# Kernel tuning notes

Measured on AMD Instinct MI355X. Metric: run time of the kernel, lower is better.

## Reference

```python
import jax, jax.numpy as jnp
import numpy as np

N_NODES = 100000
N_EDGES = 1600000
D_IN = 64
H = 64


def setup_inputs() -> dict:
    key = jax.random.key(0)
    ks = jax.random.split(key, 8)
    inp = {
        "x": jax.random.normal(ks[0], (N_NODES, D_IN), dtype=jnp.float32),
        "edge_index": jax.random.randint(ks[1], (2, N_EDGES), 0, N_NODES, dtype=jnp.int64),
        # layer 1 (SAGEConv): lin_l (aggregated neighbors, with bias), lin_r (root, no bias)
        "Wl1": jax.random.normal(ks[2], (D_IN, H), dtype=jnp.float32) / np.sqrt(D_IN),
        "bl1": jnp.zeros((H,), dtype=jnp.float32),
        "Wr1": jax.random.normal(ks[3], (D_IN, H), dtype=jnp.float32) / np.sqrt(D_IN),
        # layer 2
        "Wl2": jax.random.normal(ks[4], (H, H), dtype=jnp.float32) / np.sqrt(H),
        "bl2": jnp.zeros((H,), dtype=jnp.float32),
        "Wr2": jax.random.normal(ks[5], (H, H), dtype=jnp.float32) / np.sqrt(H),
        "Wfc": jax.random.normal(ks[6], (H, 1), dtype=jnp.float32) / np.sqrt(H),
        "bfc": jnp.zeros((1,), dtype=jnp.float32),
    }
    return inp


def _sage_conv(h, src, dst, inv_deg, Wl, bl, Wr):
    # mean-aggregate neighbor features: scatter-add messages then normalize by in-degree
    agg = jax.ops.segment_sum(h[src], dst, num_segments=N_NODES)  # [N, d]
    agg = agg * inv_deg[:, None]
    return agg @ Wl + bl + h @ Wr


def reference(x, edge_index, Wl1, bl1, Wr1, Wl2, bl2, Wr2, Wfc, bfc):
    src, dst = edge_index[0], edge_index[1]
    deg = jax.ops.segment_sum(jnp.ones((src.shape[0],), dtype=x.dtype), dst,
                              num_segments=N_NODES)
    inv_deg = jnp.where(deg > 0, 1.0 / jnp.maximum(deg, 1.0), 0.0)

    h = jax.nn.relu(_sage_conv(x, src, dst, inv_deg, Wl1, bl1, Wr1))
    h = jax.nn.relu(_sage_conv(h, src, dst, inv_deg, Wl2, bl2, Wr2))
    return h @ Wfc + bfc  # [N, 1]
```

## Files before the change

### kernel.cpp

```cpp
#include <hip/hip_runtime.h>
#include <hip/hip_fp16.h>

#define NN 100000
#define NE 1600000
#define SHIFT 8
#define NBUCK 391
#define P1B   391
#define EPB   4093

typedef _Float16 f16x8 __attribute__((ext_vector_type(8)));
typedef float f32x4 __attribute__((ext_vector_type(4)));
union H8U4 { f16x8 h; uint4 u; };

__global__ __launch_bounds__(256) void k_to_f16(const float4* __restrict__ in, ushort4* __restrict__ out, int n4) {
    int i = blockIdx.x * 256 + threadIdx.x;
    if (i < n4) {
        float4 f = in[i];
        _Float16 a = (_Float16)f.x, b = (_Float16)f.y, c = (_Float16)f.z, d = (_Float16)f.w;
        ushort4 u;
        u.x = *(unsigned short*)&a; u.y = *(unsigned short*)&b;
        u.z = *(unsigned short*)&c; u.w = *(unsigned short*)&d;
        out[i] = u;
    }
}

__global__ __launch_bounds__(256) void k_prep_w(const float* __restrict__ Wl, const float* __restrict__ Wr,
                                                unsigned short* __restrict__ wt) {
    int idx = blockIdx.x * 256 + threadIdx.x;
    if (idx < 64 * 128) {
        int n = idx >> 7, k = idx & 127;
        float v = (k < 64) ? Wl[k * 64 + n] : Wr[(k - 64) * 64 + n];
        _Float16 h = (_Float16)v;
        wt[idx] = *(unsigned short*)&h;
    }
}

__global__ __launch_bounds__(256) void k_p1_hist(const int* __restrict__ dst, int* __restrict__ hist) {
    __shared__ int h[NBUCK];
    int t = threadIdx.x, blk = blockIdx.x;
    for (int i = t; i < NBUCK; i += 256) h[i] = 0;
    __syncthreads();
    int beg = blk * EPB, end = min(beg + EPB, NE);
    for (int e = beg + t; e < end; e += 256) atomicAdd(&h[dst[e] >> SHIFT], 1);
    __syncthreads();
    for (int i = t; i < NBUCK; i += 256) hist[(size_t)i * P1B + blk] = h[i];
}

__global__ __launch_bounds__(256) void k_bin_total(const int* __restrict__ hist, int* __restrict__ bin_total) {
    __shared__ int sd[256];
    int b = blockIdx.x, t = threadIdx.x;
    int v = 0;
    for (int i = t; i < P1B; i += 256) v += hist[(size_t)b * P1B + i];
    sd[t] = v;
    __syncthreads();
    for (int s = 128; s > 0; s >>= 1) {
        if (t < s) sd[t] += sd[t + s];
        __syncthreads();
    }
    if (t == 0) bin_total[b] = sd[0];
}

__global__ __launch_bounds__(512) void k_bin_base(const int* __restrict__ bin_total, int* __restrict__ bucket_start,
                                                  int* __restrict__ offsets) {
    __shared__ int s[512];
    int t = threadIdx.x;
    int v = (t < NBUCK) ? bin_total[t] : 0;
    s[t] = v;
    __syncthreads();
    for (int off = 1; off < 512; off <<= 1) {
        int add = (t >= off) ? s[t - off] : 0;
        __syncthreads();
        s[t] += add;
        __syncthreads();
    }
    if (t < NBUCK) bucket_start[t] = s[t] - v;
    if (t == 0) { bucket_start[NBUCK] = NE; offsets[NN] = NE; }
}

__global__ __launch_bounds__(512) void k_cursor_base(int* __restrict__ hist, const int* __restrict__ bucket_start) {
    __shared__ int s[512];
    int b = blockIdx.x, t = threadIdx.x;
    int v = (t < P1B) ? hist[(size_t)b * P1B + t] : 0;
    s[t] = v;
    __syncthreads();
    for (int off = 1; off < 512; off <<= 1) {
        int add = (t >= off) ? s[t - off] : 0;
        __syncthreads();
        s[t] += add;
        __syncthreads();
    }
    if (t < P1B) hist[(size_t)b * P1B + t] = bucket_start[b] + s[t] - v;
}

__global__ __launch_bounds__(256) void k_p1_scatter(const int* __restrict__ src, const int* __restrict__ dst,
                                                    const int* __restrict__ hist, unsigned int* __restrict__ pairs) {
    __shared__ int cur[NBUCK];
    int t = threadIdx.x, blk = blockIdx.x;
    for (int i = t; i < NBUCK; i += 256) cur[i] = hist[(size_t)i * P1B + blk];
    __syncthreads();
    int beg = blk * EPB, end = min(beg + EPB, NE);
    for (int e = beg + t; e < end; e += 256) {
        int d = dst[e];
        int pos = atomicAdd(&cur[d >> SHIFT], 1);
        pairs[pos] = (unsigned int)src[e] | ((unsigned int)(d & 255) << 17);
    }
}

__global__ __launch_bounds__(256) void k_bucket_csr(const unsigned int* __restrict__ pairs,
                                                    const int* __restrict__ bucket_start,
                                                    int* __restrict__ ssrc, int* __restrict__ offsets,
                                                    float* __restrict__ inv_deg) {
    __shared__ int cnt[256];
    __shared__ int excl[256];
    int b = blockIdx.x, t = threadIdx.x;
    cnt[t] = 0;
    __syncthreads();
    int beg = bucket_start[b], end = bucket_start[b + 1];
    for (int e = beg + t; e < end; e += 256) atomicAdd(&cnt[pairs[e] >> 17], 1);
    __syncthreads();
    int deg = cnt[t];
    excl[t] = deg;
    __syncthreads();
    for (int off = 1; off < 256; off <<= 1) {
        int add = (t >= off) ? excl[t - off] : 0;
        __syncthreads();
        excl[t] += add;
        __syncthreads();
    }
    int ex = excl[t] - deg;
    int node = (b << SHIFT) + t;
    if (node < NN) {
        offsets[node] = beg + ex;
        inv_deg[node] = (deg > 0) ? (1.0f / (float)deg) : 0.0f;
    }
    __syncthreads();
    cnt[t] = beg + ex;
    __syncthreads();
    for (int e = beg + t; e < end; e += 256) {
        unsigned int pr = pairs[e];
        int pos = atomicAdd(&cnt[pr >> 17], 1);
        ssrc[pos] = (int)(pr & 0x1FFFFu);
    }
}

__global__ __launch_bounds__(256) void k_aggregate(const uint4* __restrict__ featq,
                                                   const int* __restrict__ ssrc,
                                                   const int* __restrict__ offsets, const float* __restrict__ inv_deg,
                                                   uint4* __restrict__ outq) {
    int node = blockIdx.x * 4 + (threadIdx.x >> 6);
    int lane = threadIdx.x & 63;
    if (node >= NN) return;
    int c = lane & 7, g = lane >> 3;
    int beg = offsets[node], end = offsets[node + 1];
    H8U4 acc;
    acc.h = (f16x8)(_Float16)0;
    int e = beg;

    for (; e + 16 <= end; e += 16) {
        int i0 = ssrc[e + g];
        int i1 = ssrc[e + 8 + g];
        H8U4 q0, q1;
        q0.u = featq[(size_t)i0 * 8 + c];
        q1.u = featq[(size_t)i1 * 8 + c];
        acc.h += q0.h;
        acc.h += q1.h;
    }
    for (; e < end; e += 8) {
        int m = end - e;
        int idx = ssrc[e + (g < m ? g : m - 1)];
        H8U4 q;
        q.u = featq[(size_t)idx * 8 + c];
        if (g < m) acc.h += q.h;
    }

#pragma unroll
    for (int mask = 8; mask <= 32; mask <<= 1) {
        H8U4 o;
        o.u.x = __shfl_xor(acc.u.x, mask);
        o.u.y = __shfl_xor(acc.u.y, mask);
        o.u.z = __shfl_xor(acc.u.z, mask);
        o.u.w = __shfl_xor(acc.u.w, mask);
        acc.h += o.h;
    }

    if (g == 0) {
        float s = inv_deg[node];
        H8U4 r;
#pragma unroll
        for (int j = 0; j < 8; j++) r.h[j] = (_Float16)((float)acc.h[j] * s);
        outq[(size_t)node * 8 + c] = r.u;
    }
}

template <bool FUSE_HEAD>
__global__ __launch_bounds__(256) void k_linear(const uint4* __restrict__ aggq, const uint4* __restrict__ rootq,
                                                const uint4* __restrict__ wtq,
                                                const float* __restrict__ bias,
                                                const float* __restrict__ Wfc, const float* __restrict__ bfc,
                                                float* __restrict__ out_f32, unsigned short* __restrict__ out_f16) {
    int tid = threadIdx.x;
    int wave = tid >> 6, lane = tid & 63;
    int nb = blockIdx.x * 64 + wave * 16;
    int m = lane & 15, quad = lane >> 4;

    int an = nb + m;
    if (an > NN - 1) an = NN - 1;
    H8U4 a[4];
    a[0].u = aggq[(size_t)an * 8 + quad];
    a[1].u = aggq[(size_t)an * 8 + 4 + quad];
    a[2].u = rootq[(size_t)an * 8 + quad];
    a[3].u = rootq[(size_t)an * 8 + 4 + quad];

    f32x4 acc[4];
#pragma unroll
    for (int n = 0; n < 4; n++) acc[n] = (f32x4){0.f, 0.f, 0.f, 0.f};

#pragma unroll
    for (int ncol = 0; ncol < 4; ncol++) {
        int col = ncol * 16 + m;
#pragma unroll
        for (int ki = 0; ki < 4; ki++) {
            H8U4 b;
            b.u = wtq[col * 16 + ki * 4 + quad];
            acc[ncol] = __builtin_amdgcn_mfma_f32_16x16x32_f16(a[ki].h, b.h, acc[ncol], 0, 0, 0);
        }
    }

    float bs[4];
#pragma unroll
    for (int ncol = 0; ncol < 4; ncol++) bs[ncol] = bias[ncol * 16 + m];

    if (!FUSE_HEAD) {
#pragma unroll
        for (int r = 0; r < 4; r++) {
            int node = nb + quad * 4 + r;
            if (node < NN) {
#pragma unroll
                for (int ncol = 0; ncol < 4; ncol++) {
                    float v = fmaxf(acc[ncol][r] + bs[ncol], 0.f);
                    _Float16 hv = (_Float16)v;
                    out_f16[(size_t)node * 64 + ncol * 16 + m] = *(unsigned short*)&hv;
                }
            }
        }
    } else {
        float wf[4];
#pragma unroll
        for (int ncol = 0; ncol < 4; ncol++) wf[ncol] = Wfc[ncol * 16 + m];
#pragma unroll
        for (int r = 0; r < 4; r++) {
            int node = nb + quad * 4 + r;
            float partial = 0.f;
#pragma unroll
            for (int ncol = 0; ncol < 4; ncol++)
                partial += fmaxf(acc[ncol][r] + bs[ncol], 0.f) * wf[ncol];
            partial += __shfl_xor(partial, 1);
            partial += __shfl_xor(partial, 2);
            partial += __shfl_xor(partial, 4);
            partial += __shfl_xor(partial, 8);
            if (m == 0 && node < NN) out_f32[node] = partial + bfc[0];
        }
    }
}

extern "C" void kernel_launch(void* const* d_in, const int* in_sizes, int n_in,
                              void* d_out, int out_size, void* d_ws, size_t ws_size,
                              hipStream_t stream) {
    const float* x   = (const float*)d_in[0];
    const int*   ei  = (const int*)d_in[1];
    const float* Wl1 = (const float*)d_in[2];
    const float* bl1 = (const float*)d_in[3];
    const float* Wr1 = (const float*)d_in[4];
    const float* Wl2 = (const float*)d_in[5];
    const float* bl2 = (const float*)d_in[6];
    const float* Wr2 = (const float*)d_in[7];
    const float* Wfc = (const float*)d_in[8];
    const float* bfc = (const float*)d_in[9];
    float* out = (float*)d_out;

    const int* src = ei;
    const int* dst = ei + NE;

    char* p = (char*)d_ws;
    auto carve = [&](size_t bytes) {
        char* q = p;
        p += (bytes + 255) & ~size_t(255);
        return q;
    };
    int*            offsets = (int*)carve((size_t)(NN + 1) * 4);
    float*          inv_deg = (float*)carve((size_t)NN * 4);
    int*            ssrc    = (int*)carve((size_t)NE * 4);
    unsigned short* xh      = (unsigned short*)carve((size_t)NN * 64 * 2);
    unsigned short* h1h     = (unsigned short*)carve((size_t)NN * 64 * 2);
    unsigned short* aggh    = (unsigned short*)carve((size_t)NN * 64 * 2);
    unsigned short* wt1     = (unsigned short*)carve(64 * 128 * 2);
    unsigned short* wt2     = (unsigned short*)carve(64 * 128 * 2);
    unsigned int* pairs        = (unsigned int*)aggh;
    int*          hist         = (int*)(pairs + NE);
    int*          bin_total    = hist + (size_t)NBUCK * P1B;
    int*          bucket_start = bin_total + NBUCK;

    const int n4   = NN * 64 / 4;
    const int tile = (NN + 63) / 64;

    k_to_f16<<<(n4 + 255) / 256, 256, 0, stream>>>((const float4*)x, (ushort4*)xh, n4);
    k_prep_w<<<32, 256, 0, stream>>>(Wl1, Wr1, wt1);
    k_prep_w<<<32, 256, 0, stream>>>(Wl2, Wr2, wt2);

    k_p1_hist<<<P1B, 256, 0, stream>>>(dst, hist);
    k_bin_total<<<NBUCK, 256, 0, stream>>>(hist, bin_total);
    k_bin_base<<<1, 512, 0, stream>>>(bin_total, bucket_start, offsets);
    k_cursor_base<<<NBUCK, 512, 0, stream>>>(hist, bucket_start);
    k_p1_scatter<<<P1B, 256, 0, stream>>>(src, dst, hist, pairs);
    k_bucket_csr<<<NBUCK, 256, 0, stream>>>(pairs, bucket_start, ssrc, offsets, inv_deg);

    k_aggregate<<<(NN + 3) / 4, 256, 0, stream>>>((const uint4*)xh, ssrc, offsets, inv_deg, (uint4*)aggh);
    k_linear<false><<<tile, 256, 0, stream>>>((const uint4*)aggh, (const uint4*)xh, (const uint4*)wt1,
                                              bl1, Wfc, bfc, nullptr, h1h);
    k_aggregate<<<(NN + 3) / 4, 256, 0, stream>>>((const uint4*)h1h, ssrc, offsets, inv_deg, (uint4*)aggh);
    k_linear<true><<<tile, 256, 0, stream>>>((const uint4*)aggh, (const uint4*)h1h, (const uint4*)wt2,
                                             bl2, Wfc, bfc, out, nullptr);
}
```

Baseline: 260.4 us.

## Fuse CSR build and f16 prep into one cooperative kernel with grid syncs

Replaces nine separate preprocessing launches (f16 conversion, weight transposes, histogram, bin totals, scans, scatter, bucket CSR) with a single cooperative kernel of 391 blocks that uses grid.sync between phases. The aim is to remove per-launch overhead and idle gaps between small dependent kernels. The cost is a cooperative launch that needs all 391 blocks resident at once, grid-wide barriers, and f16 conversion spread over fewer blocks, each doing a larger share.

```diff
diff --git a/kernel.cpp b/kernel.cpp
--- a/kernel.cpp
+++ b/kernel.cpp
@@ -1,5 +1,8 @@
 #include <hip/hip_runtime.h>
 #include <hip/hip_fp16.h>
+#include <hip/hip_cooperative_groups.h>
+
+namespace cg = cooperative_groups;
 
 #define NN 100000
 #define NE 1600000
@@ -12,134 +15,139 @@
 typedef float f32x4 __attribute__((ext_vector_type(4)));
 union H8U4 { f16x8 h; uint4 u; };
 
-__global__ __launch_bounds__(256) void k_to_f16(const float4* __restrict__ in, ushort4* __restrict__ out, int n4) {
-    int i = blockIdx.x * 256 + threadIdx.x;
-    if (i < n4) {
-        float4 f = in[i];
-        _Float16 a = (_Float16)f.x, b = (_Float16)f.y, c = (_Float16)f.z, d = (_Float16)f.w;
-        ushort4 u;
-        u.x = *(unsigned short*)&a; u.y = *(unsigned short*)&b;
-        u.z = *(unsigned short*)&c; u.w = *(unsigned short*)&d;
-        out[i] = u;
-    }
-}
-
-__global__ __launch_bounds__(256) void k_prep_w(const float* __restrict__ Wl, const float* __restrict__ Wr,
-                                                unsigned short* __restrict__ wt) {
-    int idx = blockIdx.x * 256 + threadIdx.x;
-    if (idx < 64 * 128) {
-        int n = idx >> 7, k = idx & 127;
-        float v = (k < 64) ? Wl[k * 64 + n] : Wr[(k - 64) * 64 + n];
-        _Float16 h = (_Float16)v;
-        wt[idx] = *(unsigned short*)&h;
-    }
-}
-
-__global__ __launch_bounds__(256) void k_p1_hist(const int* __restrict__ dst, int* __restrict__ hist) {
-    __shared__ int h[NBUCK];
-    int t = threadIdx.x, blk = blockIdx.x;
-    for (int i = t; i < NBUCK; i += 256) h[i] = 0;
-    __syncthreads();
-    int beg = blk * EPB, end = min(beg + EPB, NE);
-    for (int e = beg + t; e < end; e += 256) atomicAdd(&h[dst[e] >> SHIFT], 1);
-    __syncthreads();
-    for (int i = t; i < NBUCK; i += 256) hist[(size_t)i * P1B + blk] = h[i];
-}
-
-__global__ __launch_bounds__(256) void k_bin_total(const int* __restrict__ hist, int* __restrict__ bin_total) {
-    __shared__ int sd[256];
-    int b = blockIdx.x, t = threadIdx.x;
-    int v = 0;
-    for (int i = t; i < P1B; i += 256) v += hist[(size_t)b * P1B + i];
-    sd[t] = v;
-    __syncthreads();
-    for (int s = 128; s > 0; s >>= 1) {
-        if (t < s) sd[t] += sd[t + s];
-        __syncthreads();
-    }
-    if (t == 0) bin_total[b] = sd[0];
-}
-
-__global__ __launch_bounds__(512) void k_bin_base(const int* __restrict__ bin_total, int* __restrict__ bucket_start,
-                                                  int* __restrict__ offsets) {
-    __shared__ int s[512];
-    int t = threadIdx.x;
-    int v = (t < NBUCK) ? bin_total[t] : 0;
+__device__ __forceinline__ int scan256(int* s, int t, int v) {
     s[t] = v;
     __syncthreads();
-    for (int off = 1; off < 512; off <<= 1) {
+    for (int off = 1; off < 256; off <<= 1) {
         int add = (t >= off) ? s[t - off] : 0;
         __syncthreads();
         s[t] += add;
         __syncthreads();
     }
-    if (t < NBUCK) bucket_start[t] = s[t] - v;
-    if (t == 0) { bucket_start[NBUCK] = NE; offsets[NN] = NE; }
-}
-
-__global__ __launch_bounds__(512) void k_cursor_base(int* __restrict__ hist, const int* __restrict__ bucket_start) {
-    __shared__ int s[512];
-    int b = blockIdx.x, t = threadIdx.x;
-    int v = (t < P1B) ? hist[(size_t)b * P1B + t] : 0;
-    s[t] = v;
-    __syncthreads();
-    for (int off = 1; off < 512; off <<= 1) {
-        int add = (t >= off) ? s[t - off] : 0;
-        __syncthreads();
-        s[t] += add;
-        __syncthreads();
-    }
-    if (t < P1B) hist[(size_t)b * P1B + t] = bucket_start[b] + s[t] - v;
-}
-
-__global__ __launch_bounds__(256) void k_p1_scatter(const int* __restrict__ src, const int* __restrict__ dst,
-                                                    const int* __restrict__ hist, unsigned int* __restrict__ pairs) {
-    __shared__ int cur[NBUCK];
-    int t = threadIdx.x, blk = blockIdx.x;
-    for (int i = t; i < NBUCK; i += 256) cur[i] = hist[(size_t)i * P1B + blk];
-    __syncthreads();
-    int beg = blk * EPB, end = min(beg + EPB, NE);
-    for (int e = beg + t; e < end; e += 256) {
-        int d = dst[e];
-        int pos = atomicAdd(&cur[d >> SHIFT], 1);
-        pairs[pos] = (unsigned int)src[e] | ((unsigned int)(d & 255) << 17);
-    }
-}
-
-__global__ __launch_bounds__(256) void k_bucket_csr(const unsigned int* __restrict__ pairs,
-                                                    const int* __restrict__ bucket_start,
-                                                    int* __restrict__ ssrc, int* __restrict__ offsets,
-                                                    float* __restrict__ inv_deg) {
-    __shared__ int cnt[256];
-    __shared__ int excl[256];
-    int b = blockIdx.x, t = threadIdx.x;
-    cnt[t] = 0;
-    __syncthreads();
-    int beg = bucket_start[b], end = bucket_start[b + 1];
-    for (int e = beg + t; e < end; e += 256) atomicAdd(&cnt[pairs[e] >> 17], 1);
-    __syncthreads();
-    int deg = cnt[t];
-    excl[t] = deg;
-    __syncthreads();
-    for (int off = 1; off < 256; off <<= 1) {
-        int add = (t >= off) ? excl[t - off] : 0;
-        __syncthreads();
-        excl[t] += add;
-        __syncthreads();
-    }
-    int ex = excl[t] - deg;
-    int node = (b << SHIFT) + t;
-    if (node < NN) {
-        offsets[node] = beg + ex;
-        inv_deg[node] = (deg > 0) ? (1.0f / (float)deg) : 0.0f;
-    }
-    __syncthreads();
-    cnt[t] = beg + ex;
-    __syncthreads();
-    for (int e = beg + t; e < end; e += 256) {
-        unsigned int pr = pairs[e];
-        int pos = atomicAdd(&cnt[pr >> 17], 1);
-        ssrc[pos] = (int)(pr & 0x1FFFFu);
+    return s[t];
+}
+
+__global__ __launch_bounds__(256) void k_build(
+    const float4* __restrict__ x4, ushort4* __restrict__ xh4,
+    const float* __restrict__ Wl1, const float* __restrict__ Wr1, unsigned short* __restrict__ wt1,
+    const float* __restrict__ Wl2, const float* __restrict__ Wr2, unsigned short* __restrict__ wt2,
+    const int* __restrict__ src, const int* __restrict__ dst,
+    int* __restrict__ hist, int* __restrict__ bin_total, int* __restrict__ bucket_start,
+    unsigned int* __restrict__ pairs, int* __restrict__ ssrc,
+    int* __restrict__ offsets, float* __restrict__ inv_deg)
+{
+    cg::grid_group grid = cg::this_grid();
+    __shared__ int sA[NBUCK];
+    __shared__ int sS[256];
+    __shared__ int sX[256];
+    int blk = blockIdx.x, t = threadIdx.x;
+
+    {
+        const int n4 = NN * 16;
+        const int per = (n4 + P1B - 1) / P1B;
+        int cb = blk * per, ce = min(cb + per, n4);
+        for (int i = cb + t; i < ce; i += 256) {
+            float4 f = x4[i];
+            _Float16 a = (_Float16)f.x, b = (_Float16)f.y, c = (_Float16)f.z, d = (_Float16)f.w;
+            ushort4 u;
+            u.x = *(unsigned short*)&a; u.y = *(unsigned short*)&b;
+            u.z = *(unsigned short*)&c; u.w = *(unsigned short*)&d;
+            xh4[i] = u;
+        }
+        if (blk < 64) {
+            int idx = (blk & 31) * 256 + t;
+            const float* Wl = (blk < 32) ? Wl1 : Wl2;
+            const float* Wr = (blk < 32) ? Wr1 : Wr2;
+            unsigned short* wt = (blk < 32) ? wt1 : wt2;
+            int n = idx >> 7, k = idx & 127;
+            float v = (k < 64) ? Wl[k * 64 + n] : Wr[(k - 64) * 64 + n];
+            _Float16 h = (_Float16)v;
+            wt[idx] = *(unsigned short*)&h;
+        }
+        for (int i = t; i < NBUCK; i += 256) sA[i] = 0;
+        __syncthreads();
+        int eb = blk * EPB, ee = min(eb + EPB, NE);
+        for (int e = eb + t; e < ee; e += 256) atomicAdd(&sA[dst[e] >> SHIFT], 1);
+        __syncthreads();
+        for (int i = t; i < NBUCK; i += 256) hist[(size_t)i * P1B + blk] = sA[i];
+    }
+    grid.sync();
+
+    {
+        int v = 0;
+        for (int i = t; i < P1B; i += 256) v += hist[(size_t)blk * P1B + i];
+        sS[t] = v;
+        __syncthreads();
+        for (int s = 128; s > 0; s >>= 1) {
+            if (t < s) sS[t] += sS[t + s];
+            __syncthreads();
+        }
+        if (t == 0) bin_total[blk] = sS[0];
+    }
+    grid.sync();
+
+    if (blk == 0) {
+        int v0 = bin_total[t];
+        int incl0 = scan256(sS, t, v0);
+        bucket_start[t] = incl0 - v0;
+        __syncthreads();
+        int carry = sS[255];
+        int idx = 256 + t;
+        int v1 = (idx < NBUCK) ? bin_total[idx] : 0;
+        int incl1 = scan256(sS, t, v1);
+        if (idx < NBUCK) bucket_start[idx] = carry + incl1 - v1;
+        if (t == 0) { bucket_start[NBUCK] = NE; offsets[NN] = NE; }
+    }
+    grid.sync();
+
+    {
+        int base = bucket_start[blk];
+        int v0 = (t < P1B) ? hist[(size_t)blk * P1B + t] : 0;
+        int incl0 = scan256(sS, t, v0);
+        if (t < P1B) hist[(size_t)blk * P1B + t] = base + incl0 - v0;
+        __syncthreads();
+        int carry = sS[255];
+        int idx = 256 + t;
+        int v1 = (idx < P1B) ? hist[(size_t)blk * P1B + idx] : 0;
+        int incl1 = scan256(sS, t, v1);
+        if (idx < P1B) hist[(size_t)blk * P1B + idx] = base + carry + incl1 - v1;
+    }
+    grid.sync();
+
+    {
+        for (int i = t; i < NBUCK; i += 256) sA[i] = hist[(size_t)i * P1B + blk];
+        __syncthreads();
+        int eb = blk * EPB, ee = min(eb + EPB, NE);
+        for (int e = eb + t; e < ee; e += 256) {
+            int d = dst[e];
+            int pos = atomicAdd(&sA[d >> SHIFT], 1);
+            pairs[pos] = (unsigned int)src[e] | ((unsigned int)(d & 255) << 17);
+        }
+    }
+    grid.sync();
+
+    {
+        sX[t] = 0;
+        __syncthreads();
+        int beg = bucket_start[blk], end = bucket_start[blk + 1];
+        for (int e = beg + t; e < end; e += 256) atomicAdd(&sX[pairs[e] >> 17], 1);
+        __syncthreads();
+        int deg = sX[t];
+        int incl = scan256(sS, t, deg);
+        int ex = incl - deg;
+        int node = (blk << SHIFT) + t;
+        if (node < NN) {
+            offsets[node] = beg + ex;
+            inv_deg[node] = (deg > 0) ? (1.0f / (float)deg) : 0.0f;
+        }
+        __syncthreads();
+        sX[t] = beg + ex;
+        __syncthreads();
+        for (int e = beg + t; e < end; e += 256) {
+            unsigned int pr = pairs[e];
+            int pos = atomicAdd(&sX[pr >> 17], 1);
+            ssrc[pos] = (int)(pr & 0x1FFFFu);
+        }
     }
 }
 
@@ -278,8 +286,8 @@
     const float* bfc = (const float*)d_in[9];
     float* out = (float*)d_out;
 
-    const int* src = ei;
-    const int* dst = ei + NE;
+    const int* srcp = ei;
+    const int* dstp = ei + NE;
 
     char* p = (char*)d_ws;
     auto carve = [&](size_t bytes) {
@@ -300,19 +308,21 @@
     int*          bin_total    = hist + (size_t)NBUCK * P1B;
     int*          bucket_start = bin_total + NBUCK;
 
-    const int n4   = NN * 64 / 4;
     const int tile = (NN + 63) / 64;
 
-    k_to_f16<<<(n4 + 255) / 256, 256, 0, stream>>>((const float4*)x, (ushort4*)xh, n4);
-    k_prep_w<<<32, 256, 0, stream>>>(Wl1, Wr1, wt1);
-    k_prep_w<<<32, 256, 0, stream>>>(Wl2, Wr2, wt2);
-
-    k_p1_hist<<<P1B, 256, 0, stream>>>(dst, hist);
-    k_bin_total<<<NBUCK, 256, 0, stream>>>(hist, bin_total);
-    k_bin_base<<<1, 512, 0, stream>>>(bin_total, bucket_start, offsets);
-    k_cursor_base<<<NBUCK, 512, 0, stream>>>(hist, bucket_start);
-    k_p1_scatter<<<P1B, 256, 0, stream>>>(src, dst, hist, pairs);
-    k_bucket_csr<<<NBUCK, 256, 0, stream>>>(pairs, bucket_start, ssrc, offsets, inv_deg);
+    {
+        const float4* x4 = (const float4*)x;
+        ushort4* xh4 = (ushort4*)xh;
+        void* args[] = {
+            (void*)&x4, (void*)&xh4,
+            (void*)&Wl1, (void*)&Wr1, (void*)&wt1,
+            (void*)&Wl2, (void*)&Wr2, (void*)&wt2,
+            (void*)&srcp, (void*)&dstp,
+            (void*)&hist, (void*)&bin_total, (void*)&bucket_start,
+            (void*)&pairs, (void*)&ssrc, (void*)&offsets, (void*)&inv_deg
+        };
+        hipLaunchCooperativeKernel((void*)k_build, dim3(P1B), dim3(256), args, 0, stream);
+    }
 
     k_aggregate<<<(NN + 3) / 4, 256, 0, stream>>>((const uint4*)xh, ssrc, offsets, inv_deg, (uint4*)aggh);
     k_linear<false><<<tile, 256, 0, stream>>>((const uint4*)aggh, (const uint4*)xh, (const uint4*)wt1,
```

New measurement: 501.9 us. 92.8% more time.

## Fuse prep kernels into histogram and halve CSR bucket width

Applied to the files above, without the earlier changes.

Folds the fp16 conversion of x and both weight-transpose kernels into the histogram kernel, and merges the bucket-base scan into the cursor kernel so each block computes its own prefix by reduction. Buckets shrink from 256 to 128 nodes, doubling bucket and block counts with fewer edges per block. The goal is fewer kernel launches and more parallelism in the CSR build. In exchange the histogram matrix grows fourfold, and every cursor block redundantly sums all preceding bin totals.

```diff
diff --git a/kernel.cpp b/kernel.cpp
--- a/kernel.cpp
+++ b/kernel.cpp
@@ -3,45 +3,62 @@
 
 #define NN 100000
 #define NE 1600000
-#define SHIFT 8
-#define NBUCK 391
-#define P1B   391
-#define EPB   4093
+#define SHIFT 7
+#define NBUCK 782
+#define P1B   782
+#define EPB   2047
 
 typedef _Float16 f16x8 __attribute__((ext_vector_type(8)));
 typedef float f32x4 __attribute__((ext_vector_type(4)));
 union H8U4 { f16x8 h; uint4 u; };
 
-__global__ __launch_bounds__(256) void k_to_f16(const float4* __restrict__ in, ushort4* __restrict__ out, int n4) {
-    int i = blockIdx.x * 256 + threadIdx.x;
-    if (i < n4) {
-        float4 f = in[i];
+__device__ __forceinline__ int scan256(int* s, int t, int v) {
+    s[t] = v;
+    __syncthreads();
+    for (int off = 1; off < 256; off <<= 1) {
+        int add = (t >= off) ? s[t - off] : 0;
+        __syncthreads();
+        s[t] += add;
+        __syncthreads();
+    }
+    return s[t];
+}
+
+__global__ __launch_bounds__(256) void k_hist(
+    const float4* __restrict__ x4, ushort4* __restrict__ xh4,
+    const float* __restrict__ Wl1, const float* __restrict__ Wr1, unsigned short* __restrict__ wt1,
+    const float* __restrict__ Wl2, const float* __restrict__ Wr2, unsigned short* __restrict__ wt2,
+    const int* __restrict__ dst, int* __restrict__ hist)
+{
+    __shared__ int h[NBUCK];
+    int t = threadIdx.x, blk = blockIdx.x;
+
+    const int n4 = NN * 16;
+    const int per = (n4 + P1B - 1) / P1B;
+    int cb = blk * per, ce = min(cb + per, n4);
+    for (int i = cb + t; i < ce; i += 256) {
+        float4 f = x4[i];
         _Float16 a = (_Float16)f.x, b = (_Float16)f.y, c = (_Float16)f.z, d = (_Float16)f.w;
         ushort4 u;
         u.x = *(unsigned short*)&a; u.y = *(unsigned short*)&b;
         u.z = *(unsigned short*)&c; u.w = *(unsigned short*)&d;
-        out[i] = u;
-    }
-}
-
-__global__ __launch_bounds__(256) void k_prep_w(const float* __restrict__ Wl, const float* __restrict__ Wr,
-                                                unsigned short* __restrict__ wt) {
-    int idx = blockIdx.x * 256 + threadIdx.x;
-    if (idx < 64 * 128) {
+        xh4[i] = u;
+    }
+    if (blk < 64) {
+        int idx = (blk & 31) * 256 + t;
+        const float* Wl = (blk < 32) ? Wl1 : Wl2;
+        const float* Wr = (blk < 32) ? Wr1 : Wr2;
+        unsigned short* wt = (blk < 32) ? wt1 : wt2;
         int n = idx >> 7, k = idx & 127;
         float v = (k < 64) ? Wl[k * 64 + n] : Wr[(k - 64) * 64 + n];
-        _Float16 h = (_Float16)v;
-        wt[idx] = *(unsigned short*)&h;
-    }
-}
-
-__global__ __launch_bounds__(256) void k_p1_hist(const int* __restrict__ dst, int* __restrict__ hist) {
-    __shared__ int h[NBUCK];
-    int t = threadIdx.x, blk = blockIdx.x;
+        _Float16 hv = (_Float16)v;
+        wt[idx] = *(unsigned short*)&hv;
+    }
+
     for (int i = t; i < NBUCK; i += 256) h[i] = 0;
     __syncthreads();
-    int beg = blk * EPB, end = min(beg + EPB, NE);
-    for (int e = beg + t; e < end; e += 256) atomicAdd(&h[dst[e] >> SHIFT], 1);
+    int eb = blk * EPB, ee = min(eb + EPB, NE);
+    for (int e = eb + t; e < ee; e += 256) atomicAdd(&h[dst[e] >> SHIFT], 1);
     __syncthreads();
     for (int i = t; i < NBUCK; i += 256) hist[(size_t)i * P1B + blk] = h[i];
 }
@@ -60,49 +77,48 @@
     if (t == 0) bin_total[b] = sd[0];
 }
 
-__global__ __launch_bounds__(512) void k_bin_base(const int* __restrict__ bin_total, int* __restrict__ bucket_start,
-                                                  int* __restrict__ offsets) {
-    __shared__ int s[512];
-    int t = threadIdx.x;
-    int v = (t < NBUCK) ? bin_total[t] : 0;
-    s[t] = v;
-    __syncthreads();
-    for (int off = 1; off < 512; off <<= 1) {
-        int add = (t >= off) ? s[t - off] : 0;
-        __syncthreads();
-        s[t] += add;
-        __syncthreads();
-    }
-    if (t < NBUCK) bucket_start[t] = s[t] - v;
-    if (t == 0) { bucket_start[NBUCK] = NE; offsets[NN] = NE; }
-}
-
-__global__ __launch_bounds__(512) void k_cursor_base(int* __restrict__ hist, const int* __restrict__ bucket_start) {
-    __shared__ int s[512];
+__global__ __launch_bounds__(256) void k_cursor(int* __restrict__ hist, const int* __restrict__ bin_total,
+                                                int* __restrict__ bucket_start, int* __restrict__ offsets) {
+    __shared__ int sS[256];
     int b = blockIdx.x, t = threadIdx.x;
-    int v = (t < P1B) ? hist[(size_t)b * P1B + t] : 0;
-    s[t] = v;
-    __syncthreads();
-    for (int off = 1; off < 512; off <<= 1) {
-        int add = (t >= off) ? s[t - off] : 0;
-        __syncthreads();
-        s[t] += add;
-        __syncthreads();
-    }
-    if (t < P1B) hist[(size_t)b * P1B + t] = bucket_start[b] + s[t] - v;
-}
-
-__global__ __launch_bounds__(256) void k_p1_scatter(const int* __restrict__ src, const int* __restrict__ dst,
-                                                    const int* __restrict__ hist, unsigned int* __restrict__ pairs) {
+
+    int v = 0;
+    for (int i = t; i < b; i += 256) v += bin_total[i];
+    sS[t] = v;
+    __syncthreads();
+    for (int s = 128; s > 0; s >>= 1) {
+        if (t < s) sS[t] += sS[t + s];
+        __syncthreads();
+    }
+    int base = sS[0];
+    __syncthreads();
+    if (t == 0) bucket_start[b] = base;
+    if (b == 0 && t == 0) { bucket_start[NBUCK] = NE; offsets[NN] = NE; }
+
+    int carry = 0;
+#pragma unroll
+    for (int c = 0; c < 4; c++) {
+        int idx = c * 256 + t;
+        int hv = (idx < P1B) ? hist[(size_t)b * P1B + idx] : 0;
+        int incl = scan256(sS, t, hv);
+        if (idx < P1B) hist[(size_t)b * P1B + idx] = base + carry + incl - hv;
+        __syncthreads();
+        carry += sS[255];
+        __syncthreads();
+    }
+}
+
+__global__ __launch_bounds__(256) void k_scatter(const int* __restrict__ src, const int* __restrict__ dst,
+                                                 const int* __restrict__ hist, unsigned int* __restrict__ pairs) {
     __shared__ int cur[NBUCK];
     int t = threadIdx.x, blk = blockIdx.x;
     for (int i = t; i < NBUCK; i += 256) cur[i] = hist[(size_t)i * P1B + blk];
     __syncthreads();
-    int beg = blk * EPB, end = min(beg + EPB, NE);
-    for (int e = beg + t; e < end; e += 256) {
+    int eb = blk * EPB, ee = min(eb + EPB, NE);
+    for (int e = eb + t; e < ee; e += 256) {
         int d = dst[e];
         int pos = atomicAdd(&cur[d >> SHIFT], 1);
-        pairs[pos] = (unsigned int)src[e] | ((unsigned int)(d & 255) << 17);
+        pairs[pos] = (unsigned int)src[e] | ((unsigned int)(d & 127) << 17);
     }
 }
 
@@ -110,31 +126,24 @@
                                                     const int* __restrict__ bucket_start,
                                                     int* __restrict__ ssrc, int* __restrict__ offsets,
                                                     float* __restrict__ inv_deg) {
-    __shared__ int cnt[256];
-    __shared__ int excl[256];
+    __shared__ int cnt[128];
+    __shared__ int sS[256];
     int b = blockIdx.x, t = threadIdx.x;
-    cnt[t] = 0;
+    if (t < 128) cnt[t] = 0;
     __syncthreads();
     int beg = bucket_start[b], end = bucket_start[b + 1];
     for (int e = beg + t; e < end; e += 256) atomicAdd(&cnt[pairs[e] >> 17], 1);
     __syncthreads();
-    int deg = cnt[t];
-    excl[t] = deg;
-    __syncthreads();
-    for (int off = 1; off < 256; off <<= 1) {
-        int add = (t >= off) ? excl[t - off] : 0;
-        __syncthreads();
-        excl[t] += add;
-        __syncthreads();
-    }
-    int ex = excl[t] - deg;
+    int deg = (t < 128) ? cnt[t] : 0;
+    int incl = scan256(sS, t, deg);
+    int ex = incl - deg;
     int node = (b << SHIFT) + t;
-    if (node < NN) {
+    if (t < 128 && node < NN) {
         offsets[node] = beg + ex;
         inv_deg[node] = (deg > 0) ? (1.0f / (float)deg) : 0.0f;
     }
     __syncthreads();
-    cnt[t] = beg + ex;
+    if (t < 128) cnt[t] = beg + ex;
     __syncthreads();
     for (int e = beg + t; e < end; e += 256) {
         unsigned int pr = pairs[e];
@@ -278,8 +287,8 @@
     const float* bfc = (const float*)d_in[9];
     float* out = (float*)d_out;
 
-    const int* src = ei;
-    const int* dst = ei + NE;
+    const int* srcp = ei;
+    const int* dstp = ei + NE;
 
     char* p = (char*)d_ws;
     auto carve = [&](size_t bytes) {
@@ -300,18 +309,13 @@
     int*          bin_total    = hist + (size_t)NBUCK * P1B;
     int*          bucket_start = bin_total + NBUCK;
 
-    const int n4   = NN * 64 / 4;
     const int tile = (NN + 63) / 64;
 
-    k_to_f16<<<(n4 + 255) / 256, 256, 0, stream>>>((const float4*)x, (ushort4*)xh, n4);
-    k_prep_w<<<32, 256, 0, stream>>>(Wl1, Wr1, wt1);
-    k_prep_w<<<32, 256, 0, stream>>>(Wl2, Wr2, wt2);
-
-    k_p1_hist<<<P1B, 256, 0, stream>>>(dst, hist);
+    k_hist<<<P1B, 256, 0, stream>>>((const float4*)x, (ushort4*)xh,
+                                    Wl1, Wr1, wt1, Wl2, Wr2, wt2, dstp, hist);
     k_bin_total<<<NBUCK, 256, 0, stream>>>(hist, bin_total);
-    k_bin_base<<<1, 512, 0, stream>>>(bin_total, bucket_start, offsets);
-    k_cursor_base<<<NBUCK, 512, 0, stream>>>(hist, bucket_start);
-    k_p1_scatter<<<P1B, 256, 0, stream>>>(src, dst, hist, pairs);
+    k_cursor<<<NBUCK, 256, 0, stream>>>(hist, bin_total, bucket_start, offsets);
+    k_scatter<<<P1B, 256, 0, stream>>>(srcp, dstp, hist, pairs);
     k_bucket_csr<<<NBUCK, 256, 0, stream>>>(pairs, bucket_start, ssrc, offsets, inv_deg);
 
     k_aggregate<<<(NN + 3) / 4, 256, 0, stream>>>((const uint4*)xh, ssrc, offsets, inv_deg, (uint4*)aggh);
```

Measured after the change: 266.1 us. 1.02x slower.
